# Performance work log

Hardware: AMD Instinct MI355X
Metric: run time of the kernel (lower is better)

Reference implementation:

```python
import jax, jax.numpy as jnp
import numpy as np

B, S, D = 8, 2048, 256
H, HD = 4, 64  # num_heads, head_size; H*HD == D


def setup_inputs() -> dict:
    key = jax.random.key(0)
    ks = jax.random.split(key, 9)
    scale = 0.02
    return {
        "x": jax.random.normal(ks[0], (B, S, D), dtype=jnp.float32),
        "Wq": jax.random.normal(ks[1], (D, H * HD), dtype=jnp.float32) * scale,
        "bq": jnp.zeros((H * HD,), dtype=jnp.float32),
        "Wk": jax.random.normal(ks[2], (D, H * HD), dtype=jnp.float32) * scale,
        "bk": jnp.zeros((H * HD,), dtype=jnp.float32),
        "Wv": jax.random.normal(ks[3], (D, H * HD), dtype=jnp.float32) * scale,
        "bv": jnp.zeros((H * HD,), dtype=jnp.float32),
        "Wo": jax.random.normal(ks[4], (H * HD, D), dtype=jnp.float32) * scale,
        "bo": jnp.zeros((D,), dtype=jnp.float32),
    }


def _split_heads(t):
    # [B, S, H*HD] -> [B, H, S, HD]
    b, s, _ = t.shape
    return t.reshape(b, s, H, HD).transpose(0, 2, 1, 3)


def reference(x, Wq, bq, Wk, bk, Wv, bv, Wo, bo):
    q = _split_heads(x @ Wq + bq)
    k = _split_heads(x @ Wk + bk)
    v = _split_heads(x @ Wv + bv)
    scores = jnp.einsum("bhqd,bhkd->bhqk", q, k) / jnp.sqrt(jnp.float32(HD))
    weights = jax.nn.softmax(scores, axis=-1)
    attn = jnp.einsum("bhqk,bhkd->bhqd", weights, v)  # [B, H, S, HD]
    concat = attn.transpose(0, 2, 1, 3).reshape(x.shape[0], -1, H * HD)
    return concat @ Wo + bo
```

## Files before the change

### kernel.cpp

```cpp
#include <hip/hip_runtime.h>
#include <hip/hip_bf16.h>

namespace {

constexpr int B_ = 8, S = 2048, D = 256, H = 4, HD = 64;
constexpr int M = B_ * S;

typedef __attribute__((ext_vector_type(8))) short bf16x8;
typedef __attribute__((ext_vector_type(4))) short bf16x4;
typedef __attribute__((ext_vector_type(4))) float f32x4;
typedef __attribute__((ext_vector_type(16))) float f32x16;
typedef __attribute__((ext_vector_type(4))) unsigned uint4v;

__device__ inline short f2bf(float x) {
  __hip_bfloat16 h = __float2bfloat16(x);
  short s;
  __builtin_memcpy(&s, &h, 2);
  return s;
}

__device__ inline f32x4 mfma16(bf16x8 a, bf16x8 b, f32x4 c) {
  return __builtin_amdgcn_mfma_f32_16x16x32_bf16(a, b, c, 0, 0, 0);
}
__device__ inline f32x16 mfma32(bf16x8 a, bf16x8 b, f32x16 c) {
  return __builtin_amdgcn_mfma_f32_32x32x16_bf16(a, b, c, 0, 0, 0);
}

__device__ inline float exp2a(float x) {
  float r;
  asm("v_exp_f32 %0, %1" : "=v"(r) : "v"(x));
  return r;
}

__device__ inline unsigned cvtpk(float lo, float hi) {
  unsigned r;
  asm("v_cvt_pk_bf16_f32 %0, %1, %2" : "=v"(r) : "v"(lo), "v"(hi));
  return r;
}

__device__ inline bf16x4 pk4(float a, float b, float c, float d) {
  unsigned lo = cvtpk(a, b), hi = cvtpk(c, d);
  uint2 u{lo, hi};
  bf16x4 r;
  __builtin_memcpy(&r, &u, 8);
  return r;
}

__device__ inline bf16x8 ld_cvt8(const float* p) {
  float4 a = *(const float4*)p;
  float4 b = *(const float4*)(p + 4);
  uint4v u = {cvtpk(a.x, a.y), cvtpk(a.z, a.w), cvtpk(b.x, b.y), cvtpk(b.z, b.w)};
  bf16x8 r;
  __builtin_memcpy(&r, &u, 16);
  return r;
}

__global__ __launch_bounds__(256) void prep_w_kernel(
    const float* __restrict__ Wq, const float* __restrict__ Wk,
    const float* __restrict__ Wv, const float* __restrict__ Wo,
    short* __restrict__ WqT, short* __restrict__ WkT,
    short* __restrict__ WvT, short* __restrict__ WoT) {
  const int blk = blockIdx.x, t = threadIdx.x;
  const int wq = blk >> 4, n0 = (blk & 15) * 16;
  const float* W = wq == 0 ? Wq : wq == 1 ? Wk : wq == 2 ? Wv : Wo;
  short* Wt = wq == 0 ? WqT : wq == 1 ? WkT : wq == 2 ? WvT : WoT;
#pragma unroll
  for (int j4 = 0; j4 < 4; ++j4) {
    float4 v = *(const float4*)(W + (size_t)t * 256 + n0 + j4 * 4);
    Wt[(n0 + j4 * 4 + 0) * 256 + t] = f2bf(v.x);
    Wt[(n0 + j4 * 4 + 1) * 256 + t] = f2bf(v.y);
    Wt[(n0 + j4 * 4 + 2) * 256 + t] = f2bf(v.z);
    Wt[(n0 + j4 * 4 + 3) * 256 + t] = f2bf(v.w);
  }
}

__global__ __launch_bounds__(256) void gemm_qkv_kernel(
    const float* __restrict__ x,
    const short* __restrict__ WqT, const short* __restrict__ WkT,
    const short* __restrict__ WvT,
    const float* __restrict__ bq, const float* __restrict__ bk,
    const float* __restrict__ bv,
    short* __restrict__ Qo, short* __restrict__ Ko, short* __restrict__ Vt) {
  const int bx = blockIdx.x;
  const int which = blockIdx.y;
  const short* Wt = which == 0 ? WqT : which == 1 ? WkT : WvT;
  const float* bias = which == 0 ? bq : which == 1 ? bk : bv;

  __shared__ short Xs[2][64 * 32];
  __shared__ short Ws[2][256 * 32];

  const int tid = threadIdx.x;
  const int wid = tid >> 6, lane = tid & 63;
  const int l15 = lane & 15, l4 = lane >> 4;
  const int nt0 = wid * 4;

  const float* xsrc = x + ((size_t)(bx * 64 + (tid >> 2))) * 256 + (tid & 3) * 8;
  const short* wsrc = Wt + ((size_t)(tid >> 2)) * 256 + (tid & 3) * 8;
  short* xdst0 = &Xs[0][tid * 8];
  short* xdst1 = &Xs[1][tid * 8];
  short* wdst0 = &Ws[0][tid * 8];
  short* wdst1 = &Ws[1][tid * 8];

  bf16x8 xr, wr[4];
  xr = ld_cvt8(xsrc);
#pragma unroll
  for (int p = 0; p < 4; ++p) wr[p] = *(const bf16x8*)(wsrc + (size_t)p * 64 * 256);
  *(bf16x8*)xdst0 = xr;
#pragma unroll
  for (int p = 0; p < 4; ++p) *(bf16x8*)(wdst0 + p * 2048) = wr[p];
  __syncthreads();

  f32x4 acc[4][4];
#pragma unroll
  for (int i = 0; i < 4; ++i)
#pragma unroll
    for (int mh = 0; mh < 4; ++mh) acc[i][mh] = f32x4{0.f, 0.f, 0.f, 0.f};

  for (int ks = 0; ks < 8; ++ks) {
    const int cur = ks & 1;
    if (ks < 7) {
      xr = ld_cvt8(xsrc + (ks + 1) * 32);
#pragma unroll
      for (int p = 0; p < 4; ++p)
        wr[p] = *(const bf16x8*)(wsrc + (size_t)p * 64 * 256 + (ks + 1) * 32);
    }
    bf16x8 wf[4], xf[4];
#pragma unroll
    for (int i = 0; i < 4; ++i)
      wf[i] = *(const bf16x8*)&Ws[cur][((nt0 + i) * 16 + l15) * 32 + l4 * 8];
#pragma unroll
    for (int mh = 0; mh < 4; ++mh)
      xf[mh] = *(const bf16x8*)&Xs[cur][(mh * 16 + l15) * 32 + l4 * 8];
    if (which == 2) {
#pragma unroll
      for (int i = 0; i < 4; ++i)
#pragma unroll
        for (int mh = 0; mh < 4; ++mh)
          acc[i][mh] = mfma16(xf[mh], wf[i], acc[i][mh]);
    } else {
#pragma unroll
      for (int i = 0; i < 4; ++i)
#pragma unroll
        for (int mh = 0; mh < 4; ++mh)
          acc[i][mh] = mfma16(wf[i], xf[mh], acc[i][mh]);
    }
    if (ks < 7) {
      short* xd = (cur ? xdst0 : xdst1);
      short* wd = (cur ? wdst0 : wdst1);
      *(bf16x8*)xd = xr;
#pragma unroll
      for (int p = 0; p < 4; ++p) *(bf16x8*)(wd + p * 2048) = wr[p];
    }
    __syncthreads();
  }

  if (which == 2) {
    const int m0 = bx * 64 + l4 * 4;
#pragma unroll
    for (int i = 0; i < 4; ++i) {
      const int n = (nt0 + i) * 16 + l15;
      const float bi = bias[n];
      const int h = n >> 6, d = n & 63;
#pragma unroll
      for (int mh = 0; mh < 4; ++mh) {
        const int m = m0 + mh * 16;
        const int bb = m >> 11, s0 = m & 2047;
        bf16x4 r = pk4(acc[i][mh][0] + bi, acc[i][mh][1] + bi,
                       acc[i][mh][2] + bi, acc[i][mh][3] + bi);
        *(bf16x4*)(Vt + (((size_t)bb * H + h) * HD + d) * S + s0) = r;
      }
    }
  } else {
    const float scale = which == 0 ? 0.18033688011112042f : 1.0f;
    short* outp = which == 0 ? Qo : Ko;
#pragma unroll
    for (int i = 0; i < 4; ++i) {
      const int n0 = (nt0 + i) * 16 + l4 * 4;
      float4 bi = *(const float4*)(bias + n0);
      const int h = n0 >> 6, d0 = n0 & 63;
#pragma unroll
      for (int mh = 0; mh < 4; ++mh) {
        const int m = bx * 64 + mh * 16 + l15;
        const int bb = m >> 11, s = m & 2047;
        bf16x4 r = pk4((acc[i][mh][0] + bi.x) * scale, (acc[i][mh][1] + bi.y) * scale,
                       (acc[i][mh][2] + bi.z) * scale, (acc[i][mh][3] + bi.w) * scale);
        *(bf16x4*)(outp + (((size_t)bb * H + h) * S + s) * HD + d0) = r;
      }
    }
  }
}

__global__ __launch_bounds__(256) void gemm_out_kernel(
    const short* __restrict__ Abf, const short* __restrict__ WoT,
    const float* __restrict__ bo, float* __restrict__ out) {
  const int bx = blockIdx.x;
  __shared__ short Xs[2][64 * 32];
  __shared__ short Ws[2][256 * 32];

  const int tid = threadIdx.x;
  const int wid = tid >> 6, lane = tid & 63;
  const int l15 = lane & 15, l4 = lane >> 4;
  const int nt0 = wid * 4;

  const short* xsrc = Abf + ((size_t)(bx * 64 + (tid >> 2))) * 256 + (tid & 3) * 8;
  const short* wsrc = WoT + ((size_t)(tid >> 2)) * 256 + (tid & 3) * 8;
  short* xdst0 = &Xs[0][tid * 8];
  short* xdst1 = &Xs[1][tid * 8];
  short* wdst0 = &Ws[0][tid * 8];
  short* wdst1 = &Ws[1][tid * 8];

  bf16x8 xr, wr[4];
  xr = *(const bf16x8*)xsrc;
#pragma unroll
  for (int p = 0; p < 4; ++p) wr[p] = *(const bf16x8*)(wsrc + (size_t)p * 64 * 256);
  *(bf16x8*)xdst0 = xr;
#pragma unroll
  for (int p = 0; p < 4; ++p) *(bf16x8*)(wdst0 + p * 2048) = wr[p];
  __syncthreads();

  f32x4 acc[4][4];
#pragma unroll
  for (int i = 0; i < 4; ++i)
#pragma unroll
    for (int mh = 0; mh < 4; ++mh) acc[i][mh] = f32x4{0.f, 0.f, 0.f, 0.f};

  for (int ks = 0; ks < 8; ++ks) {
    const int cur = ks & 1;
    if (ks < 7) {
      xr = *(const bf16x8*)(xsrc + (ks + 1) * 32);
#pragma unroll
      for (int p = 0; p < 4; ++p)
        wr[p] = *(const bf16x8*)(wsrc + (size_t)p * 64 * 256 + (ks + 1) * 32);
    }
    bf16x8 wf[4], xf[4];
#pragma unroll
    for (int i = 0; i < 4; ++i)
      wf[i] = *(const bf16x8*)&Ws[cur][((nt0 + i) * 16 + l15) * 32 + l4 * 8];
#pragma unroll
    for (int mh = 0; mh < 4; ++mh)
      xf[mh] = *(const bf16x8*)&Xs[cur][(mh * 16 + l15) * 32 + l4 * 8];
#pragma unroll
    for (int i = 0; i < 4; ++i)
#pragma unroll
      for (int mh = 0; mh < 4; ++mh)
        acc[i][mh] = mfma16(wf[i], xf[mh], acc[i][mh]);
    if (ks < 7) {
      short* xd = (cur ? xdst0 : xdst1);
      short* wd = (cur ? wdst0 : wdst1);
      *(bf16x8*)xd = xr;
#pragma unroll
      for (int p = 0; p < 4; ++p) *(bf16x8*)(wd + p * 2048) = wr[p];
    }
    __syncthreads();
  }

#pragma unroll
  for (int i = 0; i < 4; ++i) {
    const int n0 = (nt0 + i) * 16 + l4 * 4;
    float4 bi = *(const float4*)(bo + n0);
#pragma unroll
    for (int mh = 0; mh < 4; ++mh) {
      const int m = bx * 64 + mh * 16 + l15;
      float4 r;
      r.x = acc[i][mh][0] + bi.x;
      r.y = acc[i][mh][1] + bi.y;
      r.z = acc[i][mh][2] + bi.z;
      r.w = acc[i][mh][3] + bi.w;
      *(float4*)(out + (size_t)m * 256 + n0) = r;
    }
  }
}

__global__ __launch_bounds__(256) void attn_kernel15(
    const short* __restrict__ Q, const short* __restrict__ K,
    const short* __restrict__ VT, short* __restrict__ Abf) {
  const int lin = blockIdx.x;
  const int bh = lin & 31;
  const int qt = lin >> 5;
  const int tid = threadIdx.x, wid = tid >> 6, lane = tid & 63;
  const int q31 = lane & 31, h = lane >> 5;
  constexpr int NT = S / 64;

  __shared__ short Ks[2][32 * 128];
  __shared__ short Vs[3][32 * 128];

  const short* Kg = K + (size_t)bh * S * HD;
  const short* Vg = VT + (size_t)bh * HD * S;
  const int qrow = qt * 128 + wid * 32;

  const short* Qg = Q + ((size_t)bh * S + qrow + q31) * HD + h * 8;
  bf16x8 qf[4];
#pragma unroll
  for (int ds = 0; ds < 4; ++ds) qf[ds] = *(const bf16x8*)(Qg + ds * 16);

  bf16x8 ones;
#pragma unroll
  for (int i = 0; i < 8; ++i) ones[i] = (short)0x3F80;

  const int srow = tid >> 2;
  const int pr = srow & 31;
  const int scol = (tid & 3) * 16;
  const int cb0 = ((srow >> 5) << 6) + scol;
  const int swz = (pr & 15) * 8;
  const int c0 = cb0 ^ swz;
  const int c1 = (cb0 + 8) ^ swz;
  const int sbase = pr * 128;

  const int fs = (q31 & 15) * 8;
  int colA[4], colB[4];
#pragma unroll
  for (int ds = 0; ds < 4; ++ds) {
    colA[ds] = (ds * 16 + h * 8) ^ fs;
    colB[ds] = (64 + ds * 16 + h * 8) ^ fs;
  }
  const int rbase = q31 * 128;

  bf16x8 kr0, kr1, vr0, vr1;
  kr0 = *(const bf16x8*)(Kg + (size_t)srow * HD + scol);
  kr1 = *(const bf16x8*)(Kg + (size_t)srow * HD + scol + 8);
  *(bf16x8*)&Ks[0][sbase + c0] = kr0;
  *(bf16x8*)&Ks[0][sbase + c1] = kr1;
  {
    const short* Kn = Kg + (size_t)64 * HD;
    kr0 = *(const bf16x8*)(Kn + (size_t)srow * HD + scol);
    kr1 = *(const bf16x8*)(Kn + (size_t)srow * HD + scol + 8);
    vr0 = *(const bf16x8*)(Vg + (size_t)srow * S + scol);
    vr1 = *(const bf16x8*)(Vg + (size_t)srow * S + scol + 8);
  }
  __syncthreads();

  f32x16 o0, o1, lsum, scA0, scA1, scB0, scB1;
#pragma unroll
  for (int i = 0; i < 16; ++i) { o0[i] = 0.f; o1[i] = 0.f; lsum[i] = 0.f; }
  bf16x8 pBA[4], pBB[4];

#define EXPPACK(S0, S1, PB)                                           \
  {                                                                   \
    _Pragma("unroll") for (int win = 0; win < 2; ++win) {             \
      const f32x16& sc = win ? (S1) : (S0);                           \
      float p[16];                                                    \
      _Pragma("unroll") for (int r = 0; r < 16; ++r)                  \
          p[r] = exp2a(sc[r]);                                        \
      unsigned w[8];                                                  \
      _Pragma("unroll") for (int i = 0; i < 8; ++i)                   \
          w[i] = cvtpk(p[2 * i], p[2 * i + 1]);                       \
      unsigned x0 = w[0], y0 = w[2], x1 = w[1], y1 = w[3];            \
      unsigned x2 = w[4], y2 = w[6], x3 = w[5], y3 = w[7];            \
      asm("v_permlane32_swap_b32 %0, %1" : "+v"(x0), "+v"(y0));       \
      asm("v_permlane32_swap_b32 %0, %1" : "+v"(x1), "+v"(y1));       \
      asm("v_permlane32_swap_b32 %0, %1" : "+v"(x2), "+v"(y2));       \
      asm("v_permlane32_swap_b32 %0, %1" : "+v"(x3), "+v"(y3));       \
      uint4v u0 = {x0, x1, y0, y1};                                   \
      uint4v u1 = {x2, x3, y2, y3};                                   \
      __builtin_memcpy(&PB[win * 2 + 0], &u0, 16);                    \
      __builtin_memcpy(&PB[win * 2 + 1], &u1, 16);                    \
    }                                                                 \
  }

#define QKBURST(KB, SCN0, SCN1)                                       \
  {                                                                   \
    _Pragma("unroll") for (int i = 0; i < 16; ++i) {                  \
      SCN0[i] = 0.f;                                                  \
      SCN1[i] = 0.f;                                                  \
    }                                                                 \
    const short* kb_ = (KB);                                          \
    _Pragma("unroll") for (int ds = 0; ds < 4; ++ds) {                \
      bf16x8 k0 = *(const bf16x8*)&kb_[rbase + colA[ds]];             \
      bf16x8 k1 = *(const bf16x8*)&kb_[rbase + colB[ds]];             \
      SCN0 = mfma32(k0, qf[ds], SCN0);                                \
      SCN1 = mfma32(k1, qf[ds], SCN1);                                \
    }                                                                 \
  }

#define PVBURST(VB, PB)                                               \
  {                                                                   \
    const short* vb_ = (VB);                                          \
    _Pragma("unroll") for (int ds = 0; ds < 4; ++ds) {                \
      bf16x8 v0 = *(const bf16x8*)&vb_[rbase + colA[ds]];             \
      bf16x8 v1 = *(const bf16x8*)&vb_[rbase + colB[ds]];             \
      o0 = mfma32(v0, PB[ds], o0);                                    \
      o1 = mfma32(v1, PB[ds], o1);                                    \
      lsum = mfma32(ones, PB[ds], lsum);                              \
    }                                                                 \
  }

#define STAGEWR(KT)                                                   \
  {                                                                   \
    if ((KT) + 1 < NT) {                                              \
      short* kw = &Ks[((KT) + 1) & 1][0];                             \
      *(bf16x8*)&kw[sbase + c0] = kr0;                                \
      *(bf16x8*)&kw[sbase + c1] = kr1;                                \
    }                                                                 \
    short* vw_ = &Vs[vw][0];                                          \
    *(bf16x8*)&vw_[sbase + c0] = vr0;                                 \
    *(bf16x8*)&vw_[sbase + c1] = vr1;                                 \
  }

#define LOADS(KT)                                                          \
  {                                                                        \
    if ((KT) + 1 < NT) {                                                   \
      const short* Kn = Kg + (size_t)((KT) + 1) * 64 * HD;                 \
      kr0 = *(const bf16x8*)(Kn + (size_t)srow * HD + scol);               \
      kr1 = *(const bf16x8*)(Kn + (size_t)srow * HD + scol + 8);           \
    }                                                                      \
    vr0 = *(const bf16x8*)(Vg + (size_t)srow * S + (KT) * 64 + scol);      \
    vr1 = *(const bf16x8*)(Vg + (size_t)srow * S + (KT) * 64 + scol + 8);  \
  }

  int vw = 0;

  {
    __builtin_amdgcn_s_setprio(1);
    QKBURST(&Ks[0][0], scA0, scA1);
    __builtin_amdgcn_s_setprio(0);
    STAGEWR(0);
    __syncthreads();
    vw = 1;
  }

  {
    LOADS(1);
    __builtin_amdgcn_s_setprio(1);
    QKBURST(&Ks[1][0], scB0, scB1);
    __builtin_amdgcn_s_setprio(0);
    EXPPACK(scA0, scA1, pBA);
    STAGEWR(1);
    __syncthreads();
    vw = 2;
  }

#define STEP(KT, SCN0, SCN1, SCP0, SCP1, PBN, PBO)                    \
  {                                                                   \
    LOADS(KT);                                                        \
    const int vr2 = (vw + 1 == 3) ? 0 : vw + 1;          \
    __builtin_amdgcn_s_setprio(1);                                    \
    QKBURST(&Ks[(KT)&1][0], SCN0, SCN1);                              \
    PVBURST(&Vs[vr2][0], PBO);                                        \
    __builtin_amdgcn_s_setprio(0);                                    \
    EXPPACK(SCP0, SCP1, PBN);                                         \
    STAGEWR(KT);                                                      \
    __syncthreads();                                                  \
    vw = (vw == 2) ? 0 : vw + 1;                                      \
  }

  for (int kt = 2; kt < NT; kt += 2) {
    STEP(kt, scA0, scA1, scB0, scB1, pBB, pBA);
    STEP(kt + 1, scB0, scB1, scA0, scA1, pBA, pBB);
  }

  {
    __builtin_amdgcn_s_setprio(1);
    PVBURST(&Vs[0][0], pBA);
    __builtin_amdgcn_s_setprio(0);
    EXPPACK(scB0, scB1, pBB);
    __builtin_amdgcn_s_setprio(1);
    PVBURST(&Vs[1][0], pBB);
    __builtin_amdgcn_s_setprio(0);
  }
#undef STEP
#undef LOADS
#undef STAGEWR
#undef PVBURST
#undef QKBURST
#undef EXPPACK

  const float inv = 1.0f / lsum[0];
  const int b = bh >> 2, hh = bh & 3;
  short* ap = Abf + ((size_t)b * S + qrow + q31) * 256 + hh * 64;
#pragma unroll
  for (int dt = 0; dt < 2; ++dt) {
    const f32x16& o = dt ? o1 : o0;
#pragma unroll
    for (int g = 0; g < 4; ++g) {
      const int d0 = dt * 32 + 8 * g + 4 * h;
      bf16x4 r = pk4(o[4 * g + 0] * inv, o[4 * g + 1] * inv,
                     o[4 * g + 2] * inv, o[4 * g + 3] * inv);
      *(bf16x4*)(ap + d0) = r;
    }
  }
}

}

extern "C" void kernel_launch(void* const* d_in, const int* in_sizes, int n_in,
                              void* d_out, int out_size, void* d_ws, size_t ws_size,
                              hipStream_t stream) {
  const float* x  = (const float*)d_in[0];
  const float* Wq = (const float*)d_in[1];
  const float* bq = (const float*)d_in[2];
  const float* Wk = (const float*)d_in[3];
  const float* bk = (const float*)d_in[4];
  const float* Wv = (const float*)d_in[5];
  const float* bv = (const float*)d_in[6];
  const float* Wo = (const float*)d_in[7];
  const float* bo = (const float*)d_in[8];
  float* out = (float*)d_out;

  const size_t per = (size_t)M * D;
  short* WqT = (short*)d_ws;
  short* WkT = WqT + 256 * 256;
  short* WvT = WkT + 256 * 256;
  short* WoT = WvT + 256 * 256;
  short* Qbf = WoT + 256 * 256;
  short* Kbf = Qbf + per;
  short* Vt  = Kbf + per;
  short* Abf = Vt + per;

  prep_w_kernel<<<64, 256, 0, stream>>>(Wq, Wk, Wv, Wo, WqT, WkT, WvT, WoT);
  gemm_qkv_kernel<<<dim3(256, 3), 256, 0, stream>>>(x, WqT, WkT, WvT, bq, bk, bv,
                                                    Qbf, Kbf, Vt);
  attn_kernel15<<<512, 256, 0, stream>>>(Qbf, Kbf, Vt, Abf);
  gemm_out_kernel<<<256, 256, 0, stream>>>(Abf, WoT, bo, out);
}
```

Before: 83.01 us.

## Load K fragments straight to registers and sum softmax denominators in VALU

The attention kernel no longer stages K tiles through shared memory. Each wave now loads its K MFMA operand fragments directly from global memory into double-buffered registers, one tile ahead. The row-sum of the exponentials is also accumulated with scalar adds during the exp pass and combined across half-waves with a shuffle, replacing the extra MFMA against a ones vector. This removes LDS writes and reads for K and one MFMA per PV step, at the cost of more VGPRs, redundant global K loads across the four waves of a block, and possibly less coalesced global access.

```diff
diff --git a/kernel.cpp b/kernel.cpp
--- a/kernel.cpp
+++ b/kernel.cpp
@@ -271,7 +271,7 @@
   }
 }
 
-__global__ __launch_bounds__(256) void attn_kernel15(
+__global__ __launch_bounds__(256) void attn_kernel16(
     const short* __restrict__ Q, const short* __restrict__ K,
     const short* __restrict__ VT, short* __restrict__ Abf) {
   const int lin = blockIdx.x;
@@ -281,7 +281,6 @@
   const int q31 = lane & 31, h = lane >> 5;
   constexpr int NT = S / 64;
 
-  __shared__ short Ks[2][32 * 128];
   __shared__ short Vs[3][32 * 128];
 
   const short* Kg = K + (size_t)bh * S * HD;
@@ -292,10 +291,6 @@
   bf16x8 qf[4];
 #pragma unroll
   for (int ds = 0; ds < 4; ++ds) qf[ds] = *(const bf16x8*)(Qg + ds * 16);
-
-  bf16x8 ones;
-#pragma unroll
-  for (int i = 0; i < 8; ++i) ones[i] = (short)0x3F80;
 
   const int srow = tid >> 2;
   const int pr = srow & 31;
@@ -315,32 +310,75 @@
   }
   const int rbase = q31 * 128;
 
-  bf16x8 kr0, kr1, vr0, vr1;
-  kr0 = *(const bf16x8*)(Kg + (size_t)srow * HD + scol);
-  kr1 = *(const bf16x8*)(Kg + (size_t)srow * HD + scol + 8);
-  *(bf16x8*)&Ks[0][sbase + c0] = kr0;
-  *(bf16x8*)&Ks[0][sbase + c1] = kr1;
-  {
-    const short* Kn = Kg + (size_t)64 * HD;
-    kr0 = *(const bf16x8*)(Kn + (size_t)srow * HD + scol);
-    kr1 = *(const bf16x8*)(Kn + (size_t)srow * HD + scol + 8);
-    vr0 = *(const bf16x8*)(Vg + (size_t)srow * S + scol);
-    vr1 = *(const bf16x8*)(Vg + (size_t)srow * S + scol + 8);
-  }
-  __syncthreads();
-
-  f32x16 o0, o1, lsum, scA0, scA1, scB0, scB1;
-#pragma unroll
-  for (int i = 0; i < 16; ++i) { o0[i] = 0.f; o1[i] = 0.f; lsum[i] = 0.f; }
-  bf16x8 pBA[4], pBB[4];
+  const short* kfp = Kg + (size_t)q31 * HD + h * 8;
+
+  f32x16 o0, o1, scA0, scA1, scB0, scB1;
+#pragma unroll
+  for (int i = 0; i < 16; ++i) { o0[i] = 0.f; o1[i] = 0.f; }
+  bf16x8 pBA[4], pBB[4], kfA[8], kfB[8];
+  bf16x8 vr0, vr1;
+  float lacc = 0.f;
+
+#define LOADKF(KT, KF)                                                \
+  {                                                                   \
+    const short* kp_ = kfp + (size_t)(KT) * 64 * HD;                  \
+    _Pragma("unroll") for (int ds = 0; ds < 4; ++ds) {                \
+      KF[ds] = *(const bf16x8*)(kp_ + ds * 16);                       \
+      KF[4 + ds] = *(const bf16x8*)(kp_ + 32 * HD + ds * 16);         \
+    }                                                                 \
+  }
+
+#define LOADV(KT)                                                          \
+  {                                                                        \
+    vr0 = *(const bf16x8*)(Vg + (size_t)srow * S + (KT) * 64 + scol);      \
+    vr1 = *(const bf16x8*)(Vg + (size_t)srow * S + (KT) * 64 + scol + 8);  \
+  }
+
+#define STAGEV()                                                      \
+  {                                                                   \
+    short* vw_ = &Vs[vw][0];                                          \
+    *(bf16x8*)&vw_[sbase + c0] = vr0;                                 \
+    *(bf16x8*)&vw_[sbase + c1] = vr1;                                 \
+  }
+
+#define QKBURST(KF, SCN0, SCN1)                                       \
+  {                                                                   \
+    _Pragma("unroll") for (int i = 0; i < 16; ++i) {                  \
+      SCN0[i] = 0.f;                                                  \
+      SCN1[i] = 0.f;                                                  \
+    }                                                                 \
+    _Pragma("unroll") for (int ds = 0; ds < 4; ++ds) {                \
+      SCN0 = mfma32(KF[ds], qf[ds], SCN0);                            \
+      SCN1 = mfma32(KF[4 + ds], qf[ds], SCN1);                        \
+    }                                                                 \
+  }
+
+#define PVBURST(VB, PB)                                               \
+  {                                                                   \
+    const short* vb_ = (VB);                                          \
+    _Pragma("unroll") for (int ds = 0; ds < 4; ++ds) {                \
+      bf16x8 v0 = *(const bf16x8*)&vb_[rbase + colA[ds]];             \
+      bf16x8 v1 = *(const bf16x8*)&vb_[rbase + colB[ds]];             \
+      o0 = mfma32(v0, PB[ds], o0);                                    \
+      o1 = mfma32(v1, PB[ds], o1);                                    \
+    }                                                                 \
+  }
 
 #define EXPPACK(S0, S1, PB)                                           \
   {                                                                   \
     _Pragma("unroll") for (int win = 0; win < 2; ++win) {             \
       const f32x16& sc = win ? (S1) : (S0);                           \
       float p[16];                                                    \
-      _Pragma("unroll") for (int r = 0; r < 16; ++r)                  \
-          p[r] = exp2a(sc[r]);                                        \
+      float a0 = 0.f, a1 = 0.f, a2 = 0.f, a3 = 0.f;                   \
+      _Pragma("unroll") for (int r = 0; r < 16; r += 4) {             \
+        p[r + 0] = exp2a(sc[r + 0]);                                  \
+        p[r + 1] = exp2a(sc[r + 1]);                                  \
+        p[r + 2] = exp2a(sc[r + 2]);                                  \
+        p[r + 3] = exp2a(sc[r + 3]);                                  \
+        a0 += p[r + 0]; a1 += p[r + 1];                               \
+        a2 += p[r + 2]; a3 += p[r + 3];                               \
+      }                                                               \
+      lacc += (a0 + a1) + (a2 + a3);                                  \
       unsigned w[8];                                                  \
       _Pragma("unroll") for (int i = 0; i < 8; ++i)                   \
           w[i] = cvtpk(p[2 * i], p[2 * i + 1]);                       \
@@ -357,95 +395,51 @@
     }                                                                 \
   }
 
-#define QKBURST(KB, SCN0, SCN1)                                       \
-  {                                                                   \
-    _Pragma("unroll") for (int i = 0; i < 16; ++i) {                  \
-      SCN0[i] = 0.f;                                                  \
-      SCN1[i] = 0.f;                                                  \
-    }                                                                 \
-    const short* kb_ = (KB);                                          \
-    _Pragma("unroll") for (int ds = 0; ds < 4; ++ds) {                \
-      bf16x8 k0 = *(const bf16x8*)&kb_[rbase + colA[ds]];             \
-      bf16x8 k1 = *(const bf16x8*)&kb_[rbase + colB[ds]];             \
-      SCN0 = mfma32(k0, qf[ds], SCN0);                                \
-      SCN1 = mfma32(k1, qf[ds], SCN1);                                \
-    }                                                                 \
-  }
-
-#define PVBURST(VB, PB)                                               \
-  {                                                                   \
-    const short* vb_ = (VB);                                          \
-    _Pragma("unroll") for (int ds = 0; ds < 4; ++ds) {                \
-      bf16x8 v0 = *(const bf16x8*)&vb_[rbase + colA[ds]];             \
-      bf16x8 v1 = *(const bf16x8*)&vb_[rbase + colB[ds]];             \
-      o0 = mfma32(v0, PB[ds], o0);                                    \
-      o1 = mfma32(v1, PB[ds], o1);                                    \
-      lsum = mfma32(ones, PB[ds], lsum);                              \
-    }                                                                 \
-  }
-
-#define STAGEWR(KT)                                                   \
-  {                                                                   \
-    if ((KT) + 1 < NT) {                                              \
-      short* kw = &Ks[((KT) + 1) & 1][0];                             \
-      *(bf16x8*)&kw[sbase + c0] = kr0;                                \
-      *(bf16x8*)&kw[sbase + c1] = kr1;                                \
-    }                                                                 \
-    short* vw_ = &Vs[vw][0];                                          \
-    *(bf16x8*)&vw_[sbase + c0] = vr0;                                 \
-    *(bf16x8*)&vw_[sbase + c1] = vr1;                                 \
-  }
-
-#define LOADS(KT)                                                          \
-  {                                                                        \
-    if ((KT) + 1 < NT) {                                                   \
-      const short* Kn = Kg + (size_t)((KT) + 1) * 64 * HD;                 \
-      kr0 = *(const bf16x8*)(Kn + (size_t)srow * HD + scol);               \
-      kr1 = *(const bf16x8*)(Kn + (size_t)srow * HD + scol + 8);           \
-    }                                                                      \
-    vr0 = *(const bf16x8*)(Vg + (size_t)srow * S + (KT) * 64 + scol);      \
-    vr1 = *(const bf16x8*)(Vg + (size_t)srow * S + (KT) * 64 + scol + 8);  \
-  }
-
   int vw = 0;
+
+  LOADKF(0, kfA);
+  LOADV(0);
 
   {
     __builtin_amdgcn_s_setprio(1);
-    QKBURST(&Ks[0][0], scA0, scA1);
+    QKBURST(kfA, scA0, scA1);
     __builtin_amdgcn_s_setprio(0);
-    STAGEWR(0);
+    LOADKF(1, kfB);
+    STAGEV();
     __syncthreads();
     vw = 1;
   }
 
   {
-    LOADS(1);
+    LOADV(1);
     __builtin_amdgcn_s_setprio(1);
-    QKBURST(&Ks[1][0], scB0, scB1);
+    QKBURST(kfB, scB0, scB1);
     __builtin_amdgcn_s_setprio(0);
     EXPPACK(scA0, scA1, pBA);
-    STAGEWR(1);
+    LOADKF(2, kfA);
+    STAGEV();
     __syncthreads();
     vw = 2;
   }
 
-#define STEP(KT, SCN0, SCN1, SCP0, SCP1, PBN, PBO)                    \
+#define STEP(KT, KFC, KFN, SCN0, SCN1, SCP0, SCP1, PBN, PBO)          \
   {                                                                   \
-    LOADS(KT);                                                        \
+    LOADV(KT);                                                        \
     const int vr2 = (vw + 1 == 3) ? 0 : vw + 1;          \
     __builtin_amdgcn_s_setprio(1);                                    \
-    QKBURST(&Ks[(KT)&1][0], SCN0, SCN1);                              \
+    QKBURST(KFC, SCN0, SCN1);                                         \
     PVBURST(&Vs[vr2][0], PBO);                                        \
     __builtin_amdgcn_s_setprio(0);                                    \
     EXPPACK(SCP0, SCP1, PBN);                                         \
-    STAGEWR(KT);                                                      \
+    if ((KT) + 1 < NT) LOADKF((KT) + 1, KFN);                         \
+    STAGEV();                                                         \
     __syncthreads();                                                  \
     vw = (vw == 2) ? 0 : vw + 1;                                      \
   }
 
   for (int kt = 2; kt < NT; kt += 2) {
-    STEP(kt, scA0, scA1, scB0, scB1, pBB, pBA);
-    STEP(kt + 1, scB0, scB1, scA0, scA1, pBA, pBB);
+    STEP(kt, kfA, kfB, scA0, scA1, scB0, scB1, pBB, pBA);
+    STEP(kt + 1, kfB, kfA, scB0, scB1, scA0, scA1, pBA, pBB);
   }
 
   {
@@ -458,13 +452,15 @@
     __builtin_amdgcn_s_setprio(0);
   }
 #undef STEP
-#undef LOADS
-#undef STAGEWR
+#undef EXPPACK
 #undef PVBURST
 #undef QKBURST
-#undef EXPPACK
-
-  const float inv = 1.0f / lsum[0];
+#undef STAGEV
+#undef LOADV
+#undef LOADKF
+
+  const float lall = lacc + __shfl_xor(lacc, 32);
+  const float inv = 1.0f / lall;
   const int b = bh >> 2, hh = bh & 3;
   short* ap = Abf + ((size_t)b * S + qrow + q31) * 256 + hh * 64;
 #pragma unroll
@@ -509,6 +505,6 @@
   prep_w_kernel<<<64, 256, 0, stream>>>(Wq, Wk, Wv, Wo, WqT, WkT, WvT, WoT);
   gemm_qkv_kernel<<<dim3(256, 3), 256, 0, stream>>>(x, WqT, WkT, WvT, bq, bk, bv,
                                                     Qbf, Kbf, Vt);
-  attn_kernel15<<<512, 256, 0, stream>>>(Qbf, Kbf, Vt, Abf);
+  attn_kernel16<<<512, 256, 0, stream>>>(Qbf, Kbf, Vt, Abf);
   gemm_out_kernel<<<256, 256, 0, stream>>>(Abf, WoT, bo, out);
 }
```

Result: slower. 127.7 us (+53.9%).

## Fuse Q/K/V projections into one GEMM block computing all 768 output columns

Applied to the files above, without the earlier changes.

The QKV projection becomes a single kernel in which each block handles 32 rows of x against all 768 concatenated Q/K/V weight columns. The old version used three grid slices that each read and converted x separately. The fp32 x tile is now loaded and converted to bf16 once per block instead of three times. In exchange, each block stages 48 KB of weights per k-step with a single-buffered weight tile and two barriers per step, uses many more registers (12x2 accumulators, 12 prefetch vectors), and writes V transposed with scalar 2-byte stores instead of 4-wide packed stores.

```diff
diff --git a/kernel.cpp b/kernel.cpp
--- a/kernel.cpp
+++ b/kernel.cpp
@@ -74,7 +74,7 @@
   }
 }
 
-__global__ __launch_bounds__(256) void gemm_qkv_kernel(
+__global__ __launch_bounds__(256) void gemm_qkv_fused(
     const float* __restrict__ x,
     const short* __restrict__ WqT, const short* __restrict__ WkT,
     const short* __restrict__ WvT,
@@ -82,108 +82,105 @@
     const float* __restrict__ bv,
     short* __restrict__ Qo, short* __restrict__ Ko, short* __restrict__ Vt) {
   const int bx = blockIdx.x;
-  const int which = blockIdx.y;
-  const short* Wt = which == 0 ? WqT : which == 1 ? WkT : WvT;
-  const float* bias = which == 0 ? bq : which == 1 ? bk : bv;
-
-  __shared__ short Xs[2][64 * 32];
-  __shared__ short Ws[2][256 * 32];
-
   const int tid = threadIdx.x;
   const int wid = tid >> 6, lane = tid & 63;
   const int l15 = lane & 15, l4 = lane >> 4;
-  const int nt0 = wid * 4;
-
-  const float* xsrc = x + ((size_t)(bx * 64 + (tid >> 2))) * 256 + (tid & 3) * 8;
-  const short* wsrc = Wt + ((size_t)(tid >> 2)) * 256 + (tid & 3) * 8;
-  short* xdst0 = &Xs[0][tid * 8];
-  short* xdst1 = &Xs[1][tid * 8];
-  short* wdst0 = &Ws[0][tid * 8];
-  short* wdst1 = &Ws[1][tid * 8];
-
-  bf16x8 xr, wr[4];
-  xr = ld_cvt8(xsrc);
-#pragma unroll
-  for (int p = 0; p < 4; ++p) wr[p] = *(const bf16x8*)(wsrc + (size_t)p * 64 * 256);
-  *(bf16x8*)xdst0 = xr;
-#pragma unroll
-  for (int p = 0; p < 4; ++p) *(bf16x8*)(wdst0 + p * 2048) = wr[p];
+
+  __shared__ short Xs[2][32 * 32];
+  __shared__ short Wall[768 * 32];
+
+  const short* wsrc[12];
+#pragma unroll
+  for (int j = 0; j < 12; ++j) {
+    const int g = j * 256 + tid;
+    const int n = g >> 2;
+    const int kc = (g & 3) * 8;
+    const short* Wp = (n < 256) ? WqT : (n < 512) ? WkT : WvT;
+    wsrc[j] = Wp + (size_t)(n & 255) * 256 + kc;
+  }
+
+  const float* xsrc = x + ((size_t)(bx * 32 + (tid >> 2))) * 256 + (tid & 3) * 8;
+  const int xoff = (tid >> 2) * 32 + (tid & 3) * 8;
+
+  bf16x8 wr[12];
+#pragma unroll
+  for (int j = 0; j < 12; ++j) wr[j] = *(const bf16x8*)(wsrc[j]);
+  bf16x8 xr;
+  if (tid < 128) xr = ld_cvt8(xsrc);
+#pragma unroll
+  for (int j = 0; j < 12; ++j)
+    *(bf16x8*)&Wall[(j * 256 + tid) * 8] = wr[j];
+  if (tid < 128) *(bf16x8*)&Xs[0][xoff] = xr;
   __syncthreads();
 
-  f32x4 acc[4][4];
-#pragma unroll
-  for (int i = 0; i < 4; ++i)
-#pragma unroll
-    for (int mh = 0; mh < 4; ++mh) acc[i][mh] = f32x4{0.f, 0.f, 0.f, 0.f};
+  f32x4 acc[12][2];
+#pragma unroll
+  for (int i = 0; i < 12; ++i) {
+    acc[i][0] = f32x4{0.f, 0.f, 0.f, 0.f};
+    acc[i][1] = f32x4{0.f, 0.f, 0.f, 0.f};
+  }
 
   for (int ks = 0; ks < 8; ++ks) {
     const int cur = ks & 1;
     if (ks < 7) {
-      xr = ld_cvt8(xsrc + (ks + 1) * 32);
-#pragma unroll
-      for (int p = 0; p < 4; ++p)
-        wr[p] = *(const bf16x8*)(wsrc + (size_t)p * 64 * 256 + (ks + 1) * 32);
-    }
-    bf16x8 wf[4], xf[4];
-#pragma unroll
-    for (int i = 0; i < 4; ++i)
-      wf[i] = *(const bf16x8*)&Ws[cur][((nt0 + i) * 16 + l15) * 32 + l4 * 8];
-#pragma unroll
-    for (int mh = 0; mh < 4; ++mh)
-      xf[mh] = *(const bf16x8*)&Xs[cur][(mh * 16 + l15) * 32 + l4 * 8];
+#pragma unroll
+      for (int j = 0; j < 12; ++j)
+        wr[j] = *(const bf16x8*)(wsrc[j] + (ks + 1) * 32);
+      if (tid < 128) xr = ld_cvt8(xsrc + (ks + 1) * 32);
+    }
+    bf16x8 xfA = *(const bf16x8*)&Xs[cur][(l15)*32 + l4 * 8];
+    bf16x8 xfB = *(const bf16x8*)&Xs[cur][(16 + l15) * 32 + l4 * 8];
+#pragma unroll
+    for (int i = 0; i < 12; ++i) {
+      bf16x8 wf = *(const bf16x8*)&Wall[((wid * 12 + i) * 16 + l15) * 32 + l4 * 8];
+      acc[i][0] = mfma16(wf, xfA, acc[i][0]);
+      acc[i][1] = mfma16(wf, xfB, acc[i][1]);
+    }
+    if (ks < 7) {
+      __syncthreads();
+#pragma unroll
+      for (int j = 0; j < 12; ++j)
+        *(bf16x8*)&Wall[(j * 256 + tid) * 8] = wr[j];
+      if (tid < 128) *(bf16x8*)&Xs[cur ^ 1][xoff] = xr;
+      __syncthreads();
+    }
+  }
+
+  const float qscale = 0.18033688011112042f;
+#pragma unroll
+  for (int i = 0; i < 12; ++i) {
+    const int n_tile = wid * 12 + i;
+    const int which = n_tile >> 4;
+    const int nbase = (n_tile & 15) * 16 + l4 * 4;
+    const int h = nbase >> 6;
     if (which == 2) {
-#pragma unroll
-      for (int i = 0; i < 4; ++i)
-#pragma unroll
-        for (int mh = 0; mh < 4; ++mh)
-          acc[i][mh] = mfma16(xf[mh], wf[i], acc[i][mh]);
+      float4 bi = *(const float4*)(bv + nbase);
+      const float bi4[4] = {bi.x, bi.y, bi.z, bi.w};
+#pragma unroll
+      for (int mh = 0; mh < 2; ++mh) {
+        const int m = bx * 32 + mh * 16 + l15;
+        const int bb = m >> 11, s = m & 2047;
+#pragma unroll
+        for (int r = 0; r < 4; ++r) {
+          const int d = (nbase + r) & 63;
+          Vt[(((size_t)bb * H + h) * HD + d) * S + s] =
+              f2bf(acc[i][mh][r] + bi4[r]);
+        }
+      }
     } else {
-#pragma unroll
-      for (int i = 0; i < 4; ++i)
-#pragma unroll
-        for (int mh = 0; mh < 4; ++mh)
-          acc[i][mh] = mfma16(wf[i], xf[mh], acc[i][mh]);
-    }
-    if (ks < 7) {
-      short* xd = (cur ? xdst0 : xdst1);
-      short* wd = (cur ? wdst0 : wdst1);
-      *(bf16x8*)xd = xr;
-#pragma unroll
-      for (int p = 0; p < 4; ++p) *(bf16x8*)(wd + p * 2048) = wr[p];
-    }
-    __syncthreads();
-  }
-
-  if (which == 2) {
-    const int m0 = bx * 64 + l4 * 4;
-#pragma unroll
-    for (int i = 0; i < 4; ++i) {
-      const int n = (nt0 + i) * 16 + l15;
-      const float bi = bias[n];
-      const int h = n >> 6, d = n & 63;
-#pragma unroll
-      for (int mh = 0; mh < 4; ++mh) {
-        const int m = m0 + mh * 16;
-        const int bb = m >> 11, s0 = m & 2047;
-        bf16x4 r = pk4(acc[i][mh][0] + bi, acc[i][mh][1] + bi,
-                       acc[i][mh][2] + bi, acc[i][mh][3] + bi);
-        *(bf16x4*)(Vt + (((size_t)bb * H + h) * HD + d) * S + s0) = r;
-      }
-    }
-  } else {
-    const float scale = which == 0 ? 0.18033688011112042f : 1.0f;
-    short* outp = which == 0 ? Qo : Ko;
-#pragma unroll
-    for (int i = 0; i < 4; ++i) {
-      const int n0 = (nt0 + i) * 16 + l4 * 4;
-      float4 bi = *(const float4*)(bias + n0);
-      const int h = n0 >> 6, d0 = n0 & 63;
-#pragma unroll
-      for (int mh = 0; mh < 4; ++mh) {
-        const int m = bx * 64 + mh * 16 + l15;
+      const float* bias = (which == 0) ? bq : bk;
+      const float scale = (which == 0) ? qscale : 1.0f;
+      short* outp = (which == 0) ? Qo : Ko;
+      float4 bi = *(const float4*)(bias + nbase);
+      const int d0 = nbase & 63;
+#pragma unroll
+      for (int mh = 0; mh < 2; ++mh) {
+        const int m = bx * 32 + mh * 16 + l15;
         const int bb = m >> 11, s = m & 2047;
-        bf16x4 r = pk4((acc[i][mh][0] + bi.x) * scale, (acc[i][mh][1] + bi.y) * scale,
-                       (acc[i][mh][2] + bi.z) * scale, (acc[i][mh][3] + bi.w) * scale);
+        bf16x4 r = pk4((acc[i][mh][0] + bi.x) * scale,
+                       (acc[i][mh][1] + bi.y) * scale,
+                       (acc[i][mh][2] + bi.z) * scale,
+                       (acc[i][mh][3] + bi.w) * scale);
         *(bf16x4*)(outp + (((size_t)bb * H + h) * S + s) * HD + d0) = r;
       }
     }
@@ -507,8 +504,8 @@
   short* Abf = Vt + per;
 
   prep_w_kernel<<<64, 256, 0, stream>>>(Wq, Wk, Wv, Wo, WqT, WkT, WvT, WoT);
-  gemm_qkv_kernel<<<dim3(256, 3), 256, 0, stream>>>(x, WqT, WkT, WvT, bq, bk, bv,
-                                                    Qbf, Kbf, Vt);
+  gemm_qkv_fused<<<512, 256, 0, stream>>>(x, WqT, WkT, WvT, bq, bk, bv,
+                                          Qbf, Kbf, Vt);
   attn_kernel15<<<512, 256, 0, stream>>>(Qbf, Kbf, Vt, Abf);
   gemm_out_kernel<<<256, 256, 0, stream>>>(Abf, WoT, bo, out);
 }
```

Measured after the change: 96.52 us. 1.16x slower.

## Split attention KV range in two and merge partial outputs in a separate kernel

Applied to the files above, without the earlier changes.

Each attention block now processes half of the key/value sequence, selected by blockIdx.y, so the attention grid doubles to 1024 blocks. Each block writes unnormalized fp32 partial outputs and row sums. A new merge kernel adds the two partials, normalizes them, converts to bf16 and writes the concatenated-head layout, reusing the Q buffer as its destination. The aim is more parallelism and better CU load balance in the attention stage. The cost is extra fp32 partial traffic to global memory and one more kernel launch.

```diff
diff --git a/kernel.cpp b/kernel.cpp
--- a/kernel.cpp
+++ b/kernel.cpp
@@ -190,6 +190,29 @@
   }
 }
 
+__global__ __launch_bounds__(256) void merge_kernel(
+    const float* __restrict__ O0, const float* __restrict__ O1,
+    const float* __restrict__ l0, const float* __restrict__ l1,
+    short* __restrict__ Abf) {
+  const size_t g = ((size_t)blockIdx.x * 256 + threadIdx.x) * 8;
+  const int bh = (int)(g >> 17);
+  const int rem = (int)(g & 131071);
+  const int q = rem >> 6, d = rem & 63;
+  const float iv = 1.0f / (l0[(size_t)bh * 2048 + q] + l1[(size_t)bh * 2048 + q]);
+  float4 a0 = *(const float4*)(O0 + g);
+  float4 a1 = *(const float4*)(O0 + g + 4);
+  float4 b0 = *(const float4*)(O1 + g);
+  float4 b1 = *(const float4*)(O1 + g + 4);
+  uint4v u = {cvtpk((a0.x + b0.x) * iv, (a0.y + b0.y) * iv),
+              cvtpk((a0.z + b0.z) * iv, (a0.w + b0.w) * iv),
+              cvtpk((a1.x + b1.x) * iv, (a1.y + b1.y) * iv),
+              cvtpk((a1.z + b1.z) * iv, (a1.w + b1.w) * iv)};
+  bf16x8 r;
+  __builtin_memcpy(&r, &u, 16);
+  const int b = bh >> 2, h = bh & 3;
+  *(bf16x8*)(Abf + ((size_t)b * 2048 + q) * 256 + h * 64 + d) = r;
+}
+
 __global__ __launch_bounds__(256) void gemm_out_kernel(
     const short* __restrict__ Abf, const short* __restrict__ WoT,
     const float* __restrict__ bo, float* __restrict__ out) {
@@ -271,21 +294,24 @@
   }
 }
 
-__global__ __launch_bounds__(256) void attn_kernel15(
+__global__ __launch_bounds__(256) void attn_kernel17(
     const short* __restrict__ Q, const short* __restrict__ K,
-    const short* __restrict__ VT, short* __restrict__ Abf) {
+    const short* __restrict__ VT, float* __restrict__ Opart,
+    float* __restrict__ lpart) {
   const int lin = blockIdx.x;
   const int bh = lin & 31;
   const int qt = lin >> 5;
+  const int sp = blockIdx.y;
   const int tid = threadIdx.x, wid = tid >> 6, lane = tid & 63;
   const int q31 = lane & 31, h = lane >> 5;
-  constexpr int NT = S / 64;
+  constexpr int NT = 16;
 
   __shared__ short Ks[2][32 * 128];
   __shared__ short Vs[3][32 * 128];
 
-  const short* Kg = K + (size_t)bh * S * HD;
+  const short* Kgs = K + (size_t)bh * S * HD + (size_t)sp * 1024 * HD;
   const short* Vg = VT + (size_t)bh * HD * S;
+  const int vcol0 = sp * 1024;
   const int qrow = qt * 128 + wid * 32;
 
   const short* Qg = Q + ((size_t)bh * S + qrow + q31) * HD + h * 8;
@@ -316,16 +342,16 @@
   const int rbase = q31 * 128;
 
   bf16x8 kr0, kr1, vr0, vr1;
-  kr0 = *(const bf16x8*)(Kg + (size_t)srow * HD + scol);
-  kr1 = *(const bf16x8*)(Kg + (size_t)srow * HD + scol + 8);
+  kr0 = *(const bf16x8*)(Kgs + (size_t)srow * HD + scol);
+  kr1 = *(const bf16x8*)(Kgs + (size_t)srow * HD + scol + 8);
   *(bf16x8*)&Ks[0][sbase + c0] = kr0;
   *(bf16x8*)&Ks[0][sbase + c1] = kr1;
   {
-    const short* Kn = Kg + (size_t)64 * HD;
+    const short* Kn = Kgs + (size_t)64 * HD;
     kr0 = *(const bf16x8*)(Kn + (size_t)srow * HD + scol);
     kr1 = *(const bf16x8*)(Kn + (size_t)srow * HD + scol + 8);
-    vr0 = *(const bf16x8*)(Vg + (size_t)srow * S + scol);
-    vr1 = *(const bf16x8*)(Vg + (size_t)srow * S + scol + 8);
+    vr0 = *(const bf16x8*)(Vg + (size_t)srow * S + vcol0 + scol);
+    vr1 = *(const bf16x8*)(Vg + (size_t)srow * S + vcol0 + scol + 8);
   }
   __syncthreads();
 
@@ -396,15 +422,15 @@
     *(bf16x8*)&vw_[sbase + c1] = vr1;                                 \
   }
 
-#define LOADS(KT)                                                          \
-  {                                                                        \
-    if ((KT) + 1 < NT) {                                                   \
-      const short* Kn = Kg + (size_t)((KT) + 1) * 64 * HD;                 \
-      kr0 = *(const bf16x8*)(Kn + (size_t)srow * HD + scol);               \
-      kr1 = *(const bf16x8*)(Kn + (size_t)srow * HD + scol + 8);           \
-    }                                                                      \
-    vr0 = *(const bf16x8*)(Vg + (size_t)srow * S + (KT) * 64 + scol);      \
-    vr1 = *(const bf16x8*)(Vg + (size_t)srow * S + (KT) * 64 + scol + 8);  \
+#define LOADS(KT)                                                              \
+  {                                                                            \
+    if ((KT) + 1 < NT) {                                                       \
+      const short* Kn = Kgs + (size_t)((KT) + 1) * 64 * HD;                    \
+      kr0 = *(const bf16x8*)(Kn + (size_t)srow * HD + scol);                   \
+      kr1 = *(const bf16x8*)(Kn + (size_t)srow * HD + scol + 8);               \
+    }                                                                          \
+    vr0 = *(const bf16x8*)(Vg + (size_t)srow * S + vcol0 + (KT) * 64 + scol);  \
+    vr1 = *(const bf16x8*)(Vg + (size_t)srow * S + vcol0 + (KT) * 64 + scol + 8); \
   }
 
   int vw = 0;
@@ -450,11 +476,11 @@
 
   {
     __builtin_amdgcn_s_setprio(1);
-    PVBURST(&Vs[0][0], pBA);
+    PVBURST(&Vs[2][0], pBA);
     __builtin_amdgcn_s_setprio(0);
     EXPPACK(scB0, scB1, pBB);
     __builtin_amdgcn_s_setprio(1);
-    PVBURST(&Vs[1][0], pBB);
+    PVBURST(&Vs[0][0], pBB);
     __builtin_amdgcn_s_setprio(0);
   }
 #undef STEP
@@ -464,19 +490,23 @@
 #undef QKBURST
 #undef EXPPACK
 
-  const float inv = 1.0f / lsum[0];
-  const int b = bh >> 2, hh = bh & 3;
-  short* ap = Abf + ((size_t)b * S + qrow + q31) * 256 + hh * 64;
+  float* op = Opart + (((size_t)sp * 32 + bh) * 2048 + qrow + q31) * 64;
 #pragma unroll
   for (int dt = 0; dt < 2; ++dt) {
     const f32x16& o = dt ? o1 : o0;
 #pragma unroll
     for (int g = 0; g < 4; ++g) {
       const int d0 = dt * 32 + 8 * g + 4 * h;
-      bf16x4 r = pk4(o[4 * g + 0] * inv, o[4 * g + 1] * inv,
-                     o[4 * g + 2] * inv, o[4 * g + 3] * inv);
-      *(bf16x4*)(ap + d0) = r;
-    }
+      float4 r;
+      r.x = o[4 * g + 0];
+      r.y = o[4 * g + 1];
+      r.z = o[4 * g + 2];
+      r.w = o[4 * g + 3];
+      *(float4*)(op + d0) = r;
+    }
+  }
+  if (lane < 32) {
+    lpart[((size_t)sp * 32 + bh) * 2048 + qrow + q31] = lsum[0];
   }
 }
 
@@ -504,11 +534,17 @@
   short* Qbf = WoT + 256 * 256;
   short* Kbf = Qbf + per;
   short* Vt  = Kbf + per;
-  short* Abf = Vt + per;
+  float* Op0 = (float*)(Vt + per);
+  float* Op1 = Op0 + per;
+  float* lp  = Op1 + per;
+  float* lp0 = lp;
+  float* lp1 = lp + 32 * 2048;
+  short* Abf = Qbf;
 
   prep_w_kernel<<<64, 256, 0, stream>>>(Wq, Wk, Wv, Wo, WqT, WkT, WvT, WoT);
   gemm_qkv_kernel<<<dim3(256, 3), 256, 0, stream>>>(x, WqT, WkT, WvT, bq, bk, bv,
                                                     Qbf, Kbf, Vt);
-  attn_kernel15<<<512, 256, 0, stream>>>(Qbf, Kbf, Vt, Abf);
+  attn_kernel17<<<dim3(512, 2), 256, 0, stream>>>(Qbf, Kbf, Vt, Op0, lp);
+  merge_kernel<<<2048, 256, 0, stream>>>(Op0, Op1, lp0, lp1, Abf);
   gemm_out_kernel<<<256, 256, 0, stream>>>(Abf, WoT, bo, out);
 }
```

Measured after the change: 91.73 us. +10.5%, slower.
